# Optimization experiments

Measured on AMD Instinct MI355X. Metric: run time of the kernel, lower is better.

## Reference

```python
import jax, jax.numpy as jnp
import numpy as np

S, M, H, E = 8192, 1024, 4096, 8
CAPACITY = S // E  # capacity_factor = 1.0, k = 1


def setup_inputs() -> dict:
    key = jax.random.key(0)
    ks = jax.random.split(key, 4)
    return {
        "x": jax.random.normal(ks[0], (S, M), jnp.float32),
        "wg": jax.random.normal(ks[1], (M, E), jnp.float32) * 0.02,
        "inter_w": jax.random.normal(ks[2], (E, M, H), jnp.float32) * 0.02,
        "inter_b": jnp.zeros((E, H), jnp.float32),
        "output_w": jax.random.normal(ks[3], (E, H, M), jnp.float32) * 0.02,
        "output_b": jnp.zeros((E, M), jnp.float32),
    }


def _top1_gate(x, wg, capacity):
    """GShard-style top-1 gate (inference: no noise, drop tokens over capacity).
    Returns combine_weights [S,E,C] (float) and dispatch_mask [S,E,C] (float 0/1)."""
    logits = x @ wg                                   # [S,E]
    gates = jax.nn.softmax(logits, axis=-1)           # [S,E]
    idx = jnp.argmax(gates, axis=-1)                  # [S]
    mask1 = jax.nn.one_hot(idx, gates.shape[-1], dtype=gates.dtype)  # [S,E]
    # 0-based position of each token within its expert's queue
    locations = jnp.cumsum(mask1, axis=0) - mask1     # [S,E]
    mask1 = mask1 * (locations < capacity)            # drop overflow tokens
    pos = jnp.sum(locations * mask1, axis=1).astype(jnp.int32)  # [S]
    gate_s = jnp.sum(gates * mask1, axis=1)           # [S] gate value of kept tokens
    loc_oh = jax.nn.one_hot(pos, capacity, dtype=gates.dtype)    # [S,C]
    combine = gate_s[:, None, None] * mask1[:, :, None] * loc_oh[:, None, :]  # [S,E,C]
    dispatch = (combine > 0).astype(x.dtype)
    return combine, dispatch


def reference(x, wg, inter_w, inter_b, output_w, output_b):
    combine, dispatch = _top1_gate(x, wg, CAPACITY)
    # token dispatch: torch.einsum('sec,sm->ecm', dispatch_mask, attention_output)
    disp_x = jnp.einsum('sec,sm->ecm', dispatch, x)                 # [E,C,M]
    # per-expert fused gelu-GEMM MLP (gelu_gemm_func: gelu(x@W1+b1)@W2, +b2)
    h = jax.nn.gelu(jnp.einsum('ecm,emh->ech', disp_x, inter_w)
                    + inter_b[:, None, :], approximate=False)       # [E,C,H]
    exp_out = jnp.einsum('ech,ehm->ecm', h, output_w) + output_b[:, None, :]  # [E,C,M]
    # combine: combined_weights.reshape(S, E*C) @ expert_output.reshape(E*C, M)
    y = jnp.einsum('sec,ecm->sm', combine, exp_out)                 # [S,M]
    return y
```

## Files before the change

kernel.cpp:

```cpp
#include <hip/hip_runtime.h>

#define S_ 8192
#define M_ 1024
#define H_ 4096
#define E_ 8
#define C_ 1024

typedef short s16x8 __attribute__((ext_vector_type(8)));
typedef float f32x4 __attribute__((ext_vector_type(4)));

__device__ __forceinline__ unsigned short f2bf(float f) {
    unsigned int u = __float_as_uint(f);
    unsigned int r = u + 0x7fffu + ((u >> 16) & 1u);
    return (unsigned short)(r >> 16);
}

__device__ __forceinline__ void async_copy16(const unsigned short* g, unsigned short* l) {
    __builtin_amdgcn_global_load_lds(
        (const __attribute__((address_space(1))) unsigned int*)g,
        (__attribute__((address_space(3))) unsigned int*)l, 16, 0, 0);
}

__global__ __launch_bounds__(256) void gate_kernel(
    const float* __restrict__ x, const float* __restrict__ wg,
    int* __restrict__ expert_of, float* __restrict__ gate_full,
    unsigned short* __restrict__ xb)
{
    int token = (blockIdx.x * 256 + threadIdx.x) >> 6;
    int lane  = threadIdx.x & 63;
    const float* xr = x + (size_t)token * M_;
    unsigned short* xbr = xb + (size_t)token * M_;
    double acc[E_] = {0,0,0,0,0,0,0,0};
    for (int t = 0; t < M_ / 64; ++t) {
        int m = t * 64 + lane;
        float xf = xr[m];
        xbr[m] = f2bf(xf);
        double xv = (double)xf;
        const float* w = wg + m * E_;
        #pragma unroll
        for (int e = 0; e < E_; ++e) acc[e] += xv * (double)w[e];
    }
    #pragma unroll
    for (int e = 0; e < E_; ++e)
        for (int off = 32; off; off >>= 1) acc[e] += __shfl_xor(acc[e], off);
    if (lane == 0) {
        double mx = acc[0]; int idx = 0;
        #pragma unroll
        for (int e = 1; e < E_; ++e) if (acc[e] > mx) { mx = acc[e]; idx = e; }
        double den = 0.0;
        #pragma unroll
        for (int e = 0; e < E_; ++e) den += exp(acc[e] - mx);
        expert_of[token] = idx;
        gate_full[token] = (float)(1.0 / den);
    }
}

__global__ __launch_bounds__(256) void scan_kernel(
    const int* __restrict__ expert_of, int* __restrict__ slot_to_token)
{
    __shared__ int wave_cnt[4][E_];
    __shared__ int base_[E_];
    int tid = threadIdx.x, lane = tid & 63, wv = tid >> 6;
    for (int i = tid; i < E_ * C_; i += 256) slot_to_token[i] = -1;
    if (tid < E_) base_[tid] = 0;
    __syncthreads();
    for (int chunk = 0; chunk < S_ / 256; ++chunk) {
        int s = chunk * 256 + tid;
        int e = expert_of[s];
        unsigned long long mymask = 0;
        #pragma unroll
        for (int j = 0; j < E_; ++j) {
            unsigned long long b = __ballot(e == j);
            if (lane == 0) wave_cnt[wv][j] = __popcll(b);
            if (j == e) mymask = b;
        }
        __syncthreads();
        int wave_off = 0;
        for (int w2 = 0; w2 < wv; ++w2) wave_off += wave_cnt[w2][e];
        int pos = base_[e] + wave_off +
                  __popcll(mymask & ((1ull << lane) - 1ull));
        __syncthreads();
        if (tid < E_) {
            int hsum = 0;
            #pragma unroll
            for (int w2 = 0; w2 < 4; ++w2) hsum += wave_cnt[w2][tid];
            base_[tid] += hsum;
        }
        if (pos < C_) slot_to_token[e * C_ + pos] = s;
        __syncthreads();
    }
}

__global__ __launch_bounds__(256) void transpose_cvt_kernel(
    const float* __restrict__ src, unsigned short* __restrict__ dst,
    int K, int N, int e_base)
{
    __shared__ unsigned short tile[64 * 84];
    const size_t esz = (size_t)K * N;
    const float* s = src + (size_t)(e_base + blockIdx.z) * esz;
    unsigned short* d = dst + (size_t)blockIdx.z * esz;
    const int k0 = blockIdx.y * 64, n0 = blockIdx.x * 64;
    const int tid = threadIdx.x;
    {
        const int n  = tid & 63;
        const int kb = (tid >> 6) * 16;
        #pragma unroll
        for (int i = 0; i < 4; ++i) {
            int k4 = kb + i * 4;
            float a0 = s[(size_t)(k0 + k4 + 0) * N + n0 + n];
            float a1 = s[(size_t)(k0 + k4 + 1) * N + n0 + n];
            float a2 = s[(size_t)(k0 + k4 + 2) * N + n0 + n];
            float a3 = s[(size_t)(k0 + k4 + 3) * N + n0 + n];
            unsigned long long p = (unsigned long long)f2bf(a0)
                | ((unsigned long long)f2bf(a1) << 16)
                | ((unsigned long long)f2bf(a2) << 32)
                | ((unsigned long long)f2bf(a3) << 48);
            *(unsigned long long*)(&tile[n * 84 + k4]) = p;
        }
    }
    __syncthreads();
    {
        const int n  = tid >> 3;
        const int k8 = (tid & 7) * 8;
        #pragma unroll
        for (int j = 0; j < 2; ++j) {
            int nn = n + j * 32;
            unsigned long long lo = *(const unsigned long long*)(&tile[nn * 84 + k8]);
            unsigned long long hi = *(const unsigned long long*)(&tile[nn * 84 + k8 + 4]);
            ulonglong2 v; v.x = lo; v.y = hi;
            *(ulonglong2*)(d + (size_t)(n0 + nn) * K + k0 + k8) = v;
        }
    }
}

__global__ __launch_bounds__(256) void gemm1_kernel(
    const unsigned short* __restrict__ xb, const unsigned short* __restrict__ w1t,
    const float* __restrict__ b1, const int* __restrict__ slot_to_token,
    unsigned short* __restrict__ h, int e_base)
{
    const int eloc = blockIdx.z;
    const int e    = e_base + eloc;
    const int n0 = blockIdx.x * 128;
    const int c0 = blockIdx.y * 128;

    __shared__ unsigned short As[128 * 32];
    __shared__ unsigned short Bs[128 * 32];
    __shared__ int tok[128];

    const int tid = threadIdx.x;
    if (tid < 128) tok[tid] = slot_to_token[e * C_ + c0 + tid];
    __syncthreads();

    const int q0 = tid, q1 = 256 + tid;
    const int r0 = q0 >> 2, cq0 = q0 & 3;
    const int r1 = q1 >> 2, cq1 = q1 & 3;
    int t0 = tok[r0]; if (t0 < 0) t0 = 0;
    int t1 = tok[r1]; if (t1 < 0) t1 = 0;
    const unsigned short* srcA0 = xb + (size_t)t0 * M_ + cq0 * 8;
    const unsigned short* srcA1 = xb + (size_t)t1 * M_ + cq1 * 8;
    const unsigned short* Bp = w1t + (size_t)eloc * M_ * H_;
    const unsigned short* srcB0 = Bp + (size_t)(n0 + r0) * M_ + cq0 * 8;
    const unsigned short* srcB1 = Bp + (size_t)(n0 + r1) * M_ + cq1 * 8;
    const int wave = tid >> 6;
    unsigned short* dstA0 = As + wave * 512;
    unsigned short* dstA1 = As + 2048 + wave * 512;
    unsigned short* dstB0 = Bs + wave * 512;
    unsigned short* dstB1 = Bs + 2048 + wave * 512;

    f32x4 acc[4][4] = {};
    const int lane = tid & 63;
    const int wr = wave >> 1, wc = wave & 1;
    const int qd = lane >> 4, ln16 = lane & 15;

    for (int k0 = 0; k0 < M_; k0 += 32) {
        async_copy16(srcA0 + k0, dstA0);
        async_copy16(srcA1 + k0, dstA1);
        async_copy16(srcB0 + k0, dstB0);
        async_copy16(srcB1 + k0, dstB1);
        __syncthreads();
        s16x8 af[4], bfr[4];
        #pragma unroll
        for (int i = 0; i < 4; ++i) {
            int m = wr * 64 + i * 16 + ln16;
            af[i] = *(const s16x8*)(&As[m * 32 + qd * 8]);
        }
        #pragma unroll
        for (int j = 0; j < 4; ++j) {
            int n = wc * 64 + j * 16 + ln16;
            bfr[j] = *(const s16x8*)(&Bs[n * 32 + qd * 8]);
        }
        #pragma unroll
        for (int i = 0; i < 4; ++i)
            #pragma unroll
            for (int j = 0; j < 4; ++j)
                acc[i][j] = __builtin_amdgcn_mfma_f32_16x16x32_bf16(
                    af[i], bfr[j], acc[i][j], 0, 0, 0);
        __syncthreads();
    }

    unsigned short* hb = h + (size_t)eloc * C_ * H_;
    #pragma unroll
    for (int i = 0; i < 4; ++i) {
        #pragma unroll
        for (int j = 0; j < 4; ++j) {
            int n = n0 + wc * 64 + j * 16 + ln16;
            float bias = b1[e * H_ + n];
            #pragma unroll
            for (int r = 0; r < 4; ++r) {
                int c = c0 + wr * 64 + i * 16 + qd * 4 + r;
                float v = acc[i][j][r] + bias;
                float g = 0.5f * v * (1.0f + erff(v * 0.70710678118f));
                hb[(size_t)c * H_ + n] = f2bf(g);
            }
        }
    }
}

__global__ __launch_bounds__(256) void gemm2_kernel(
    const unsigned short* __restrict__ h, const unsigned short* __restrict__ w2t,
    const float* __restrict__ b2, const int* __restrict__ slot_to_token,
    const float* __restrict__ gate_full, float* __restrict__ y, int e_base)
{
    const int eloc = blockIdx.z;
    const int e    = e_base + eloc;
    const int n0 = blockIdx.x * 128;
    const int c0 = blockIdx.y * 128;

    __shared__ unsigned short As[128 * 32];
    __shared__ unsigned short Bs[128 * 32];
    __shared__ int tok[128];

    const int tid = threadIdx.x;
    if (tid < 128) tok[tid] = slot_to_token[e * C_ + c0 + tid];
    __syncthreads();

    const int q0 = tid, q1 = 256 + tid;
    const int r0 = q0 >> 2, cq0 = q0 & 3;
    const int r1 = q1 >> 2, cq1 = q1 & 3;
    const unsigned short* Ap = h + (size_t)eloc * C_ * H_;
    const unsigned short* srcA0 = Ap + (size_t)(c0 + r0) * H_ + cq0 * 8;
    const unsigned short* srcA1 = Ap + (size_t)(c0 + r1) * H_ + cq1 * 8;
    const unsigned short* Bp = w2t + (size_t)eloc * H_ * M_;
    const unsigned short* srcB0 = Bp + (size_t)(n0 + r0) * H_ + cq0 * 8;
    const unsigned short* srcB1 = Bp + (size_t)(n0 + r1) * H_ + cq1 * 8;
    const int wave = tid >> 6;
    unsigned short* dstA0 = As + wave * 512;
    unsigned short* dstA1 = As + 2048 + wave * 512;
    unsigned short* dstB0 = Bs + wave * 512;
    unsigned short* dstB1 = Bs + 2048 + wave * 512;

    f32x4 acc[4][4] = {};
    const int lane = tid & 63;
    const int wr = wave >> 1, wc = wave & 1;
    const int qd = lane >> 4, ln16 = lane & 15;

    for (int k0 = 0; k0 < H_; k0 += 32) {
        async_copy16(srcA0 + k0, dstA0);
        async_copy16(srcA1 + k0, dstA1);
        async_copy16(srcB0 + k0, dstB0);
        async_copy16(srcB1 + k0, dstB1);
        __syncthreads();
        s16x8 af[4], bfr[4];
        #pragma unroll
        for (int i = 0; i < 4; ++i) {
            int m = wr * 64 + i * 16 + ln16;
            af[i] = *(const s16x8*)(&As[m * 32 + qd * 8]);
        }
        #pragma unroll
        for (int j = 0; j < 4; ++j) {
            int n = wc * 64 + j * 16 + ln16;
            bfr[j] = *(const s16x8*)(&Bs[n * 32 + qd * 8]);
        }
        #pragma unroll
        for (int i = 0; i < 4; ++i)
            #pragma unroll
            for (int j = 0; j < 4; ++j)
                acc[i][j] = __builtin_amdgcn_mfma_f32_16x16x32_bf16(
                    af[i], bfr[j], acc[i][j], 0, 0, 0);
        __syncthreads();
    }

    #pragma unroll
    for (int i = 0; i < 4; ++i) {
        #pragma unroll
        for (int r = 0; r < 4; ++r) {
            int c = wr * 64 + i * 16 + qd * 4 + r;
            int t = tok[c];
            if (t < 0) continue;
            float g = gate_full[t];
            float* yr = y + (size_t)t * M_;
            #pragma unroll
            for (int j = 0; j < 4; ++j) {
                int n = n0 + wc * 64 + j * 16 + ln16;
                yr[n] = g * (acc[i][j][r] + b2[e * M_ + n]);
            }
        }
    }
}

extern "C" void kernel_launch(void* const* d_in, const int* in_sizes, int n_in,
                              void* d_out, int out_size, void* d_ws, size_t ws_size,
                              hipStream_t stream) {
    const float* x  = (const float*)d_in[0];
    const float* wg = (const float*)d_in[1];
    const float* w1 = (const float*)d_in[2];
    const float* b1 = (const float*)d_in[3];
    const float* w2 = (const float*)d_in[4];
    const float* b2 = (const float*)d_in[5];
    float* y = (float*)d_out;

    char* ws = (char*)d_ws;
    int*   expert_of     = (int*)ws;
    int*   slot_to_token = (int*)(ws + 32768);
    float* gate_full     = (float*)(ws + 65536);
    unsigned short* xb   = (unsigned short*)(ws + 98304);

    const size_t xb_bytes = (size_t)S_ * M_ * 2;
    const size_t per_e    = (size_t)M_ * H_ * 2;
    size_t base = 98304 + xb_bytes;
    size_t avail = (ws_size > base) ? ws_size - base : 0;
    int ec = (int)(avail / (3 * per_e));
    if (ec < 1) ec = 1;
    if (ec > E_) ec = E_;

    unsigned short* h   = (unsigned short*)(ws + base);
    unsigned short* w1t = h   + (size_t)ec * C_ * H_;
    unsigned short* w2t = w1t + (size_t)ec * M_ * H_;

    hipMemsetAsync(d_out, 0, (size_t)S_ * M_ * sizeof(float), stream);
    gate_kernel<<<S_ / 4, 256, 0, stream>>>(x, wg, expert_of, gate_full, xb);
    scan_kernel<<<1, 256, 0, stream>>>(expert_of, slot_to_token);

    for (int e0 = 0; e0 < E_; e0 += ec) {
        int cnt = (E_ - e0 < ec) ? (E_ - e0) : ec;
        transpose_cvt_kernel<<<dim3(H_ / 64, M_ / 64, cnt), 256, 0, stream>>>(
            w1, w1t, M_, H_, e0);
        gemm1_kernel<<<dim3(H_ / 128, C_ / 128, cnt), 256, 0, stream>>>(
            xb, w1t, b1, slot_to_token, h, e0);
        transpose_cvt_kernel<<<dim3(M_ / 64, H_ / 64, cnt), 256, 0, stream>>>(
            w2, w2t, H_, M_, e0);
        gemm2_kernel<<<dim3(M_ / 128, C_ / 128, cnt), 256, 0, stream>>>(
            h, w2t, b2, slot_to_token, gate_full, y, e0);
    }
}
```

Baseline: 602.8 us.

## Parallelize scan, enlarge GEMM tiles, split-K gemm2 with separate combine

The single-block serial scan is replaced by parallel count, prefix and scatter kernels. Both GEMMs now use 256x128 tiles with 8x4 MFMA accumulators per wave and a launch bound of two blocks per CU. gemm2 splits K into four chunks so the grid is larger, writes bf16 partial sums, and a new combine kernel reduces them and applies bias and gate. Weight-transpose buffers are shared and the expert chunk size is fixed at four. The split-K path adds extra partial-sum traffic, and storing the partials in bf16 costs some precision.

```diff
diff --git a/kernel.cpp b/kernel.cpp
--- a/kernel.cpp
+++ b/kernel.cpp
@@ -5,6 +5,7 @@
 #define H_ 4096
 #define E_ 8
 #define C_ 1024
+#define EC_ 4
 
 typedef short s16x8 __attribute__((ext_vector_type(8)));
 typedef float f32x4 __attribute__((ext_vector_type(4)));
@@ -13,6 +14,9 @@
     unsigned int u = __float_as_uint(f);
     unsigned int r = u + 0x7fffu + ((u >> 16) & 1u);
     return (unsigned short)(r >> 16);
+}
+__device__ __forceinline__ float bf2f(unsigned short s) {
+    return __uint_as_float(((unsigned int)s) << 16);
 }
 
 __device__ __forceinline__ void async_copy16(const unsigned short* g, unsigned short* l) {
@@ -55,40 +59,59 @@
     }
 }
 
-__global__ __launch_bounds__(256) void scan_kernel(
-    const int* __restrict__ expert_of, int* __restrict__ slot_to_token)
-{
-    __shared__ int wave_cnt[4][E_];
-    __shared__ int base_[E_];
+__global__ __launch_bounds__(256) void count_kernel(
+    const int* __restrict__ expert_of, int* __restrict__ cnt,
+    int* __restrict__ slot_to_token)
+{
+    __shared__ int wc[4][E_];
     int tid = threadIdx.x, lane = tid & 63, wv = tid >> 6;
-    for (int i = tid; i < E_ * C_; i += 256) slot_to_token[i] = -1;
-    if (tid < E_) base_[tid] = 0;
+    slot_to_token[blockIdx.x * 256 + tid] = -1;
+    int e = expert_of[blockIdx.x * 256 + tid];
+    #pragma unroll
+    for (int j = 0; j < E_; ++j) {
+        unsigned long long b = __ballot(e == j);
+        if (lane == 0) wc[wv][j] = __popcll(b);
+    }
     __syncthreads();
-    for (int chunk = 0; chunk < S_ / 256; ++chunk) {
-        int s = chunk * 256 + tid;
-        int e = expert_of[s];
-        unsigned long long mymask = 0;
-        #pragma unroll
-        for (int j = 0; j < E_; ++j) {
-            unsigned long long b = __ballot(e == j);
-            if (lane == 0) wave_cnt[wv][j] = __popcll(b);
-            if (j == e) mymask = b;
-        }
-        __syncthreads();
-        int wave_off = 0;
-        for (int w2 = 0; w2 < wv; ++w2) wave_off += wave_cnt[w2][e];
-        int pos = base_[e] + wave_off +
-                  __popcll(mymask & ((1ull << lane) - 1ull));
-        __syncthreads();
-        if (tid < E_) {
-            int hsum = 0;
-            #pragma unroll
-            for (int w2 = 0; w2 < 4; ++w2) hsum += wave_cnt[w2][tid];
-            base_[tid] += hsum;
-        }
-        if (pos < C_) slot_to_token[e * C_ + pos] = s;
-        __syncthreads();
-    }
+    if (tid < E_) {
+        int s = 0;
+        #pragma unroll
+        for (int w = 0; w < 4; ++w) s += wc[w][tid];
+        cnt[blockIdx.x * E_ + tid] = s;
+    }
+}
+
+__global__ __launch_bounds__(64) void prefix_kernel(
+    const int* __restrict__ cnt, int* __restrict__ cbase)
+{
+    int tid = threadIdx.x;
+    if (tid < E_) {
+        int run = 0;
+        for (int b = 0; b < 32; ++b) { cbase[b * E_ + tid] = run; run += cnt[b * E_ + tid]; }
+    }
+}
+
+__global__ __launch_bounds__(256) void scatter_kernel(
+    const int* __restrict__ expert_of, const int* __restrict__ cbase,
+    int* __restrict__ slot_to_token)
+{
+    __shared__ int wc[4][E_];
+    int tid = threadIdx.x, lane = tid & 63, wv = tid >> 6;
+    int s = blockIdx.x * 256 + tid;
+    int e = expert_of[s];
+    unsigned long long mymask = 0;
+    #pragma unroll
+    for (int j = 0; j < E_; ++j) {
+        unsigned long long b = __ballot(e == j);
+        if (lane == 0) wc[wv][j] = __popcll(b);
+        if (j == e) mymask = b;
+    }
+    __syncthreads();
+    int waveoff = 0;
+    for (int w = 0; w < 4; ++w) if (w < wv) waveoff += wc[w][e];
+    int pos = cbase[blockIdx.x * E_ + e] + waveoff +
+              __popcll(mymask & ((1ull << lane) - 1ull));
+    if (pos < C_) slot_to_token[e * C_ + pos] = s;
 }
 
 __global__ __launch_bounds__(256) void transpose_cvt_kernel(
@@ -133,64 +156,56 @@
     }
 }
 
-__global__ __launch_bounds__(256) void gemm1_kernel(
+__global__ __launch_bounds__(256, 2) void gemm1_kernel(
     const unsigned short* __restrict__ xb, const unsigned short* __restrict__ w1t,
     const float* __restrict__ b1, const int* __restrict__ slot_to_token,
     unsigned short* __restrict__ h, int e_base)
 {
-    const int eloc = blockIdx.z;
-    const int e    = e_base + eloc;
-    const int n0 = blockIdx.x * 128;
-    const int c0 = blockIdx.y * 128;
-
-    __shared__ unsigned short As[128 * 32];
+    const int eloc = blockIdx.z, e = e_base + eloc;
+    const int n0 = blockIdx.x * 128, c0 = blockIdx.y * 256;
+    __shared__ unsigned short As[256 * 32];
     __shared__ unsigned short Bs[128 * 32];
-    __shared__ int tok[128];
-
+    __shared__ int tok[256];
     const int tid = threadIdx.x;
-    if (tid < 128) tok[tid] = slot_to_token[e * C_ + c0 + tid];
+    tok[tid] = slot_to_token[e * C_ + c0 + tid];
     __syncthreads();
-
-    const int q0 = tid, q1 = 256 + tid;
-    const int r0 = q0 >> 2, cq0 = q0 & 3;
-    const int r1 = q1 >> 2, cq1 = q1 & 3;
-    int t0 = tok[r0]; if (t0 < 0) t0 = 0;
-    int t1 = tok[r1]; if (t1 < 0) t1 = 0;
-    const unsigned short* srcA0 = xb + (size_t)t0 * M_ + cq0 * 8;
-    const unsigned short* srcA1 = xb + (size_t)t1 * M_ + cq1 * 8;
+    const int wave = tid >> 6, lane = tid & 63;
+
+    const unsigned short* srcA[4]; unsigned short* dstA[4];
+    #pragma unroll
+    for (int s = 0; s < 4; ++s) {
+        int q = s * 256 + tid, r = q >> 2, cq = q & 3;
+        int t = tok[r]; if (t < 0) t = 0;
+        srcA[s] = xb + (size_t)t * M_ + cq * 8;
+        dstA[s] = As + s * 2048 + wave * 512;
+    }
     const unsigned short* Bp = w1t + (size_t)eloc * M_ * H_;
-    const unsigned short* srcB0 = Bp + (size_t)(n0 + r0) * M_ + cq0 * 8;
-    const unsigned short* srcB1 = Bp + (size_t)(n0 + r1) * M_ + cq1 * 8;
-    const int wave = tid >> 6;
-    unsigned short* dstA0 = As + wave * 512;
-    unsigned short* dstA1 = As + 2048 + wave * 512;
-    unsigned short* dstB0 = Bs + wave * 512;
-    unsigned short* dstB1 = Bs + 2048 + wave * 512;
-
-    f32x4 acc[4][4] = {};
-    const int lane = tid & 63;
-    const int wr = wave >> 1, wc = wave & 1;
-    const int qd = lane >> 4, ln16 = lane & 15;
+    const unsigned short* srcB[2]; unsigned short* dstB[2];
+    #pragma unroll
+    for (int s = 0; s < 2; ++s) {
+        int q = s * 256 + tid, r = q >> 2, cq = q & 3;
+        srcB[s] = Bp + (size_t)(n0 + r) * M_ + cq * 8;
+        dstB[s] = Bs + s * 2048 + wave * 512;
+    }
+
+    f32x4 acc[8][4] = {};
+    const int wr = wave >> 1, wc = wave & 1, qd = lane >> 4, ln16 = lane & 15;
 
     for (int k0 = 0; k0 < M_; k0 += 32) {
-        async_copy16(srcA0 + k0, dstA0);
-        async_copy16(srcA1 + k0, dstA1);
-        async_copy16(srcB0 + k0, dstB0);
-        async_copy16(srcB1 + k0, dstB1);
+        #pragma unroll
+        for (int s = 0; s < 4; ++s) async_copy16(srcA[s] + k0, dstA[s]);
+        #pragma unroll
+        for (int s = 0; s < 2; ++s) async_copy16(srcB[s] + k0, dstB[s]);
         __syncthreads();
-        s16x8 af[4], bfr[4];
-        #pragma unroll
-        for (int i = 0; i < 4; ++i) {
-            int m = wr * 64 + i * 16 + ln16;
-            af[i] = *(const s16x8*)(&As[m * 32 + qd * 8]);
-        }
-        #pragma unroll
-        for (int j = 0; j < 4; ++j) {
-            int n = wc * 64 + j * 16 + ln16;
-            bfr[j] = *(const s16x8*)(&Bs[n * 32 + qd * 8]);
-        }
-        #pragma unroll
-        for (int i = 0; i < 4; ++i)
+        s16x8 af[8], bfr[4];
+        #pragma unroll
+        for (int i = 0; i < 8; ++i)
+            af[i] = *(const s16x8*)(&As[(wr * 128 + i * 16 + ln16) * 32 + qd * 8]);
+        #pragma unroll
+        for (int j = 0; j < 4; ++j)
+            bfr[j] = *(const s16x8*)(&Bs[(wc * 64 + j * 16 + ln16) * 32 + qd * 8]);
+        #pragma unroll
+        for (int i = 0; i < 8; ++i)
             #pragma unroll
             for (int j = 0; j < 4; ++j)
                 acc[i][j] = __builtin_amdgcn_mfma_f32_16x16x32_bf16(
@@ -200,79 +215,69 @@
 
     unsigned short* hb = h + (size_t)eloc * C_ * H_;
     #pragma unroll
-    for (int i = 0; i < 4; ++i) {
+    for (int i = 0; i < 8; ++i) {
+        int crow = c0 + wr * 128 + i * 16 + qd * 4;
         #pragma unroll
         for (int j = 0; j < 4; ++j) {
             int n = n0 + wc * 64 + j * 16 + ln16;
             float bias = b1[e * H_ + n];
             #pragma unroll
             for (int r = 0; r < 4; ++r) {
-                int c = c0 + wr * 64 + i * 16 + qd * 4 + r;
                 float v = acc[i][j][r] + bias;
                 float g = 0.5f * v * (1.0f + erff(v * 0.70710678118f));
-                hb[(size_t)c * H_ + n] = f2bf(g);
+                hb[(size_t)(crow + r) * H_ + n] = f2bf(g);
             }
         }
     }
 }
 
-__global__ __launch_bounds__(256) void gemm2_kernel(
+__global__ __launch_bounds__(256, 2) void gemm2_kernel(
     const unsigned short* __restrict__ h, const unsigned short* __restrict__ w2t,
-    const float* __restrict__ b2, const int* __restrict__ slot_to_token,
-    const float* __restrict__ gate_full, float* __restrict__ y, int e_base)
-{
-    const int eloc = blockIdx.z;
-    const int e    = e_base + eloc;
-    const int n0 = blockIdx.x * 128;
-    const int c0 = blockIdx.y * 128;
-
-    __shared__ unsigned short As[128 * 32];
+    unsigned short* __restrict__ part)
+{
+    const int eloc = blockIdx.z >> 2, kc = blockIdx.z & 3;
+    const int n0 = blockIdx.x * 128, c0 = blockIdx.y * 256;
+    const int kb = kc * 1024;
+    __shared__ unsigned short As[256 * 32];
     __shared__ unsigned short Bs[128 * 32];
-    __shared__ int tok[128];
-
     const int tid = threadIdx.x;
-    if (tid < 128) tok[tid] = slot_to_token[e * C_ + c0 + tid];
-    __syncthreads();
-
-    const int q0 = tid, q1 = 256 + tid;
-    const int r0 = q0 >> 2, cq0 = q0 & 3;
-    const int r1 = q1 >> 2, cq1 = q1 & 3;
+    const int wave = tid >> 6, lane = tid & 63;
+
     const unsigned short* Ap = h + (size_t)eloc * C_ * H_;
-    const unsigned short* srcA0 = Ap + (size_t)(c0 + r0) * H_ + cq0 * 8;
-    const unsigned short* srcA1 = Ap + (size_t)(c0 + r1) * H_ + cq1 * 8;
-    const unsigned short* Bp = w2t + (size_t)eloc * H_ * M_;
-    const unsigned short* srcB0 = Bp + (size_t)(n0 + r0) * H_ + cq0 * 8;
-    const unsigned short* srcB1 = Bp + (size_t)(n0 + r1) * H_ + cq1 * 8;
-    const int wave = tid >> 6;
-    unsigned short* dstA0 = As + wave * 512;
-    unsigned short* dstA1 = As + 2048 + wave * 512;
-    unsigned short* dstB0 = Bs + wave * 512;
-    unsigned short* dstB1 = Bs + 2048 + wave * 512;
-
-    f32x4 acc[4][4] = {};
-    const int lane = tid & 63;
-    const int wr = wave >> 1, wc = wave & 1;
-    const int qd = lane >> 4, ln16 = lane & 15;
-
-    for (int k0 = 0; k0 < H_; k0 += 32) {
-        async_copy16(srcA0 + k0, dstA0);
-        async_copy16(srcA1 + k0, dstA1);
-        async_copy16(srcB0 + k0, dstB0);
-        async_copy16(srcB1 + k0, dstB1);
+    const unsigned short* Bp = w2t + (size_t)eloc * M_ * H_;
+    const unsigned short* srcA[4]; unsigned short* dstA[4];
+    #pragma unroll
+    for (int s = 0; s < 4; ++s) {
+        int q = s * 256 + tid, r = q >> 2, cq = q & 3;
+        srcA[s] = Ap + (size_t)(c0 + r) * H_ + kb + cq * 8;
+        dstA[s] = As + s * 2048 + wave * 512;
+    }
+    const unsigned short* srcB[2]; unsigned short* dstB[2];
+    #pragma unroll
+    for (int s = 0; s < 2; ++s) {
+        int q = s * 256 + tid, r = q >> 2, cq = q & 3;
+        srcB[s] = Bp + (size_t)(n0 + r) * H_ + kb + cq * 8;
+        dstB[s] = Bs + s * 2048 + wave * 512;
+    }
+
+    f32x4 acc[8][4] = {};
+    const int wr = wave >> 1, wc = wave & 1, qd = lane >> 4, ln16 = lane & 15;
+
+    for (int k0 = 0; k0 < 1024; k0 += 32) {
+        #pragma unroll
+        for (int s = 0; s < 4; ++s) async_copy16(srcA[s] + k0, dstA[s]);
+        #pragma unroll
+        for (int s = 0; s < 2; ++s) async_copy16(srcB[s] + k0, dstB[s]);
         __syncthreads();
-        s16x8 af[4], bfr[4];
-        #pragma unroll
-        for (int i = 0; i < 4; ++i) {
-            int m = wr * 64 + i * 16 + ln16;
-            af[i] = *(const s16x8*)(&As[m * 32 + qd * 8]);
-        }
-        #pragma unroll
-        for (int j = 0; j < 4; ++j) {
-            int n = wc * 64 + j * 16 + ln16;
-            bfr[j] = *(const s16x8*)(&Bs[n * 32 + qd * 8]);
-        }
-        #pragma unroll
-        for (int i = 0; i < 4; ++i)
+        s16x8 af[8], bfr[4];
+        #pragma unroll
+        for (int i = 0; i < 8; ++i)
+            af[i] = *(const s16x8*)(&As[(wr * 128 + i * 16 + ln16) * 32 + qd * 8]);
+        #pragma unroll
+        for (int j = 0; j < 4; ++j)
+            bfr[j] = *(const s16x8*)(&Bs[(wc * 64 + j * 16 + ln16) * 32 + qd * 8]);
+        #pragma unroll
+        for (int i = 0; i < 8; ++i)
             #pragma unroll
             for (int j = 0; j < 4; ++j)
                 acc[i][j] = __builtin_amdgcn_mfma_f32_16x16x32_bf16(
@@ -280,21 +285,50 @@
         __syncthreads();
     }
 
-    #pragma unroll
-    for (int i = 0; i < 4; ++i) {
-        #pragma unroll
-        for (int r = 0; r < 4; ++r) {
-            int c = wr * 64 + i * 16 + qd * 4 + r;
-            int t = tok[c];
-            if (t < 0) continue;
-            float g = gate_full[t];
-            float* yr = y + (size_t)t * M_;
+    unsigned short* pp = part + ((size_t)(kc * EC_ + eloc) * C_) * M_;
+    #pragma unroll
+    for (int i = 0; i < 8; ++i) {
+        int crow = c0 + wr * 128 + i * 16 + qd * 4;
+        #pragma unroll
+        for (int j = 0; j < 4; ++j) {
+            int n = n0 + wc * 64 + j * 16 + ln16;
             #pragma unroll
-            for (int j = 0; j < 4; ++j) {
-                int n = n0 + wc * 64 + j * 16 + ln16;
-                yr[n] = g * (acc[i][j][r] + b2[e * M_ + n]);
-            }
-        }
+            for (int r = 0; r < 4; ++r)
+                pp[(size_t)(crow + r) * M_ + n] = f2bf(acc[i][j][r]);
+        }
+    }
+}
+
+__global__ __launch_bounds__(256) void combine_kernel(
+    const unsigned short* __restrict__ part, const float* __restrict__ b2,
+    const int* __restrict__ slot_to_token, const float* __restrict__ gate_full,
+    float* __restrict__ y, int e_base)
+{
+    const int sid  = blockIdx.x * 4 + (threadIdx.x >> 6);
+    const int lane = threadIdx.x & 63;
+    const int eloc = sid >> 10, c = sid & 1023;
+    const int t = slot_to_token[(e_base + eloc) * C_ + c];
+    if (t < 0) return;
+    const float g = gate_full[t];
+    float* yr = y + (size_t)t * M_;
+    const float* b2r = b2 + (e_base + eloc) * M_;
+    #pragma unroll
+    for (int v = 0; v < 4; ++v) {
+        int n = v * 256 + lane * 4;
+        float sum0 = 0.f, sum1 = 0.f, sum2 = 0.f, sum3 = 0.f;
+        #pragma unroll
+        for (int kc = 0; kc < 4; ++kc) {
+            const unsigned short* pr =
+                part + ((size_t)(kc * EC_ + eloc) * C_ + c) * M_ + n;
+            ushort4 u = *(const ushort4*)pr;
+            sum0 += bf2f(u.x); sum1 += bf2f(u.y);
+            sum2 += bf2f(u.z); sum3 += bf2f(u.w);
+        }
+        float4 bb = *(const float4*)(b2r + n);
+        float4 o;
+        o.x = g * (sum0 + bb.x); o.y = g * (sum1 + bb.y);
+        o.z = g * (sum2 + bb.z); o.w = g * (sum3 + bb.w);
+        *(float4*)(yr + n) = o;
     }
 }
 
@@ -310,36 +344,32 @@
     float* y = (float*)d_out;
 
     char* ws = (char*)d_ws;
-    int*   expert_of     = (int*)ws;
-    int*   slot_to_token = (int*)(ws + 32768);
-    float* gate_full     = (float*)(ws + 65536);
+    int*   slot_to_token = (int*)ws;
+    float* gate_full     = (float*)(ws + 32768);
+    int*   cnt           = (int*)(ws + 65536);
+    int*   cbase         = (int*)(ws + 66560);
     unsigned short* xb   = (unsigned short*)(ws + 98304);
-
-    const size_t xb_bytes = (size_t)S_ * M_ * 2;
-    const size_t per_e    = (size_t)M_ * H_ * 2;
-    size_t base = 98304 + xb_bytes;
-    size_t avail = (ws_size > base) ? ws_size - base : 0;
-    int ec = (int)(avail / (3 * per_e));
-    if (ec < 1) ec = 1;
-    if (ec > E_) ec = E_;
-
-    unsigned short* h   = (unsigned short*)(ws + base);
-    unsigned short* w1t = h   + (size_t)ec * C_ * H_;
-    unsigned short* w2t = w1t + (size_t)ec * M_ * H_;
+    unsigned short* h    = xb + (size_t)S_ * M_;
+    unsigned short* wt   = h + (size_t)EC_ * C_ * H_;
+    unsigned short* part = wt + (size_t)EC_ * M_ * H_;
+    int* expert_of = (int*)part;
 
     hipMemsetAsync(d_out, 0, (size_t)S_ * M_ * sizeof(float), stream);
     gate_kernel<<<S_ / 4, 256, 0, stream>>>(x, wg, expert_of, gate_full, xb);
-    scan_kernel<<<1, 256, 0, stream>>>(expert_of, slot_to_token);
-
-    for (int e0 = 0; e0 < E_; e0 += ec) {
-        int cnt = (E_ - e0 < ec) ? (E_ - e0) : ec;
-        transpose_cvt_kernel<<<dim3(H_ / 64, M_ / 64, cnt), 256, 0, stream>>>(
-            w1, w1t, M_, H_, e0);
-        gemm1_kernel<<<dim3(H_ / 128, C_ / 128, cnt), 256, 0, stream>>>(
-            xb, w1t, b1, slot_to_token, h, e0);
-        transpose_cvt_kernel<<<dim3(M_ / 64, H_ / 64, cnt), 256, 0, stream>>>(
-            w2, w2t, H_, M_, e0);
-        gemm2_kernel<<<dim3(M_ / 128, C_ / 128, cnt), 256, 0, stream>>>(
-            h, w2t, b2, slot_to_token, gate_full, y, e0);
-    }
-}
+    count_kernel<<<32, 256, 0, stream>>>(expert_of, cnt, slot_to_token);
+    prefix_kernel<<<1, 64, 0, stream>>>(cnt, cbase);
+    scatter_kernel<<<32, 256, 0, stream>>>(expert_of, cbase, slot_to_token);
+
+    for (int e0 = 0; e0 < E_; e0 += EC_) {
+        transpose_cvt_kernel<<<dim3(H_ / 64, M_ / 64, EC_), 256, 0, stream>>>(
+            w1, wt, M_, H_, e0);
+        gemm1_kernel<<<dim3(H_ / 128, C_ / 256, EC_), 256, 0, stream>>>(
+            xb, wt, b1, slot_to_token, h, e0);
+        transpose_cvt_kernel<<<dim3(M_ / 64, H_ / 64, EC_), 256, 0, stream>>>(
+            w2, wt, H_, M_, e0);
+        gemm2_kernel<<<dim3(M_ / 128, C_ / 256, EC_ * 4), 256, 0, stream>>>(
+            h, wt, part);
+        combine_kernel<<<1024, 256, 0, stream>>>(
+            part, b2, slot_to_token, gate_full, y, e0);
+    }
+}
```

After: 583.8 us. -3.1%, faster.
